# Kernel tuning notes

Hardware: AMD Instinct MI355X
Metric: run time of the kernel (lower is better)

Reference implementation:

```python
import jax, jax.numpy as jnp
import numpy as np

N = 100000
C = 64
E = 3200000


def setup_inputs() -> dict:
    key = jax.random.key(0)
    k1, k2, k3 = jax.random.split(key, 3)
    edge_index = jax.random.randint(k1, (2, E), 0, N, dtype=jnp.int64)
    # nn.Linear(num_nodes, out_channels): weight [C, N], bias [C]
    W = jax.random.normal(k2, (C, N), dtype=jnp.float32) * 0.01
    b = jax.random.normal(k3, (C,), dtype=jnp.float32) * 0.01
    return {"edge_index": edge_index, "W": W, "b": b}


def reference(edge_index, W, b):
    # logits = A @ W.T + b, with A the N x N COO adjacency built from edge_index.
    # Row r of A @ W.T = sum_{edges (r, c)} W[:, c], so this is a gather of
    # W.T rows at col, segment-summed over row (duplicate edges accumulate,
    # matching torch sparse COO semantics).
    n = W.shape[1]
    row = edge_index[0]
    col = edge_index[1]
    row = row - row.min()  # faithful to the original's row normalization
    Wt = W.T  # [N, C]
    gathered = Wt[col]  # [E, C]
    out = jax.ops.segment_sum(gathered, row, num_segments=n)  # [N, C]
    return out + b
```

## Files before the change

### kernel.cpp

```cpp
#include <hip/hip_runtime.h>


#define OVF_MAX (1 << 19)
#define NBKT_MAX 400
#define SLOTS 36
#define FLUSH_T 24
#define GT_STRIDE 16
#define SL 64

__device__ __forceinline__ float bf16u_to_f(unsigned short u) {
    union { unsigned int i; float f; } x; x.i = ((unsigned int)u) << 16; return x.f;
}

__global__ __launch_bounds__(1024) void LINK_detect_kernel(
    const unsigned int* __restrict__ words, int E, int* __restrict__ flags,
    int* __restrict__ gtail, int nbkt, int segcap) {
    long long twoE = 2LL * E;
    int tid = threadIdx.x;
    unsigned int oddOr = 0u;
    int nscan = (int)(twoE < 8192 ? twoE : 8192);
    for (int i = tid; i < nscan; i += blockDim.x) {
        if (i & 1) oddOr |= words[i];
        long long j = twoE - 1 - i;
        if (j >= nscan && (j & 1)) oddOr |= words[j];
    }
    __shared__ unsigned int sred[16];
    for (int off = 32; off > 0; off >>= 1)
        oddOr |= (unsigned int)__shfl_down((int)oddOr, off, 64);
    int wid = tid >> 6;
    if ((tid & 63) == 0) sred[wid] = oddOr;
    __syncthreads();
    if (tid == 0) {
        unsigned int o = 0;
        for (int i = 0; i < (int)(blockDim.x >> 6); ++i) o |= sred[i];
        flags[0] = o ? 1 : 0;
        flags[1] = 0x7fffffff;
        flags[8] = 0;
    }
    for (int k = tid; k < nbkt; k += blockDim.x) gtail[k * GT_STRIDE] = k * segcap;
}

__global__ void LINK_transpose_kernel(const float* __restrict__ W,
                                      unsigned short* __restrict__ Wtb, int N) {
    __shared__ float tile[64][65];
    int n0 = blockIdx.x * 64;
    int lx = threadIdx.x & 63;
    int ly = threadIdx.x >> 6;
#pragma unroll
    for (int it = 0; it < 16; ++it) {
        int ch = ly + 4 * it;
        float v = 0.0f;
        if (n0 + lx < N) v = W[(size_t)ch * N + (n0 + lx)];
        tile[lx][ch] = v;
    }
    __syncthreads();
#pragma unroll
    for (int it = 0; it < 16; ++it) {
        int nn = ly + 4 * it;
        if (n0 + nn < N) {
            union { float f; unsigned int i; } x; x.f = tile[nn][lx];
            unsigned int u = x.i;
            unsigned int r = (u + 0x7fffu + ((u >> 16) & 1u)) >> 16;
            Wtb[((size_t)(n0 + nn) << 6) + lx] = (unsigned short)r;
        }
    }
}

__global__ __launch_bounds__(1024) void LINK_part_kernel(
    const unsigned int* __restrict__ words, int E, int N, int nbkt, int segcap,
    int* __restrict__ gtail, unsigned int* __restrict__ recs,
    int* __restrict__ ovf, int* __restrict__ flags) {
    __shared__ unsigned int lstage[NBKT_MAX * SLOTS];
    __shared__ int lcnt[NBKT_MAX];
    __shared__ int sred[16];
    int tid = threadIdx.x;
    for (int k = tid; k < nbkt; k += blockDim.x) lcnt[k] = 0;
    __syncthreads();
    int isInt32 = flags[0];
    int mnr = 0x7fffffff;
    int nblk = gridDim.x;
    long long per_round = (long long)nblk * blockDim.x;
    long long nround = ((long long)E + per_round - 1) / per_round;
    int lane = tid & 63, wid = tid >> 6, nw = blockDim.x >> 6;
    for (long long rd = 0; rd < nround; ++rd) {
        long long e = (rd * nblk + blockIdx.x) * blockDim.x + tid;
        if (e < E) {
            int r, c;
            if (isInt32) {
                r = (int)__builtin_nontemporal_load(words + e);
                c = (int)__builtin_nontemporal_load(words + E + e);
            } else {
                r = (int)__builtin_nontemporal_load(words + 2 * e);
                c = (int)__builtin_nontemporal_load(words + 2LL * E + 2 * e);
            }
            mnr = min(mnr, r);
            if ((unsigned)r < (unsigned)N && (unsigned)c < (unsigned)N) {
                int k = r >> 8;
                unsigned int rec = ((unsigned int)(r & 255) << 17) | (unsigned int)c;
                int pos = atomicAdd(&lcnt[k], 1);
                if (pos < SLOTS) {
                    lstage[k * SLOTS + pos] = rec;
                } else {
                    int g = atomicAdd(&gtail[k * GT_STRIDE], 1);
                    if (g < (k + 1) * segcap) recs[g] = rec;
                    else {
                        int oi = atomicAdd(&flags[8], 1);
                        if (oi < OVF_MAX) { ovf[2 * oi] = r; ovf[2 * oi + 1] = c; }
                    }
                }
            }
        }
        __syncthreads();
        bool last = (rd == nround - 1);
        for (int k = wid; k < nbkt; k += nw) {
            int cnt = lcnt[k]; if (cnt > SLOTS) cnt = SLOTS;
            if (cnt >= FLUSH_T || (last && cnt > 0)) {
                int g = 0;
                if (lane == 0) g = atomicAdd(&gtail[k * GT_STRIDE], cnt);
                g = __shfl(g, 0);
                if (lane < cnt) {
                    int gg = g + lane;
                    unsigned int rec = lstage[k * SLOTS + lane];
                    if (gg < (k + 1) * segcap) recs[gg] = rec;
                    else {
                        int oi = atomicAdd(&flags[8], 1);
                        if (oi < OVF_MAX) {
                            ovf[2 * oi] = (k << 8) | (int)(rec >> 17);
                            ovf[2 * oi + 1] = (int)(rec & 0x1FFFF);
                        }
                    }
                }
                if (lane == 0) lcnt[k] = 0;
            }
        }
        __syncthreads();
    }
    for (int off = 32; off > 0; off >>= 1) mnr = min(mnr, __shfl_down(mnr, off, 64));
    if (lane == 0) sred[wid] = mnr;
    __syncthreads();
    if (tid == 0) {
        int m = 0x7fffffff;
        for (int i = 0; i < 16; ++i) m = min(m, sred[i]);
        atomicMin(&flags[1], m);
    }
}

__global__ __launch_bounds__(256, 8) void LINK_bgather_kernel(
    const int* __restrict__ gtail, const unsigned int* __restrict__ recs, int segcap,
    const unsigned short* __restrict__ Wtb, const float* __restrict__ bias,
    float* __restrict__ out, int* __restrict__ flags, int* __restrict__ ovf, int N) {
    __shared__ int lcols[64 * SL];
    __shared__ int lcnt[64];
    int b = blockIdx.x >> 2;
    int sub = blockIdx.x & 3;
    int tid = threadIdx.x;
    if (tid < 64) lcnt[tid] = 0;
    __syncthreads();
    int len = gtail[b * GT_STRIDE] - b * segcap;
    if (len > segcap) len = segcap;
    if (len < 0) len = 0;
    const unsigned int* rp = recs + (size_t)b * segcap;
    for (int i = tid; i < len; i += 256) {
        unsigned int rec = rp[i];
        int lrf = (int)(rec >> 17);
        if ((lrf >> 6) != sub) continue;
        int lr = lrf & 63;
        int c = (int)(rec & 0x1FFFF);
        int pos = atomicAdd(&lcnt[lr], 1);
        if (pos < SL) {
            lcols[(lr << 6) + pos] = c;
        } else {
            int oi = atomicAdd(&flags[8], 1);
            if (oi < OVF_MAX) { ovf[2 * oi] = (b << 8) | lrf; ovf[2 * oi + 1] = c; }
        }
    }
    __syncthreads();
    int rmin = flags[1];
    int lane = tid & 63, wid = tid >> 6;
    for (int lr = wid; lr < 64; lr += 4) {
        int cnt = lcnt[lr]; if (cnt > SL) cnt = SL;
        int base = lr << 6;
        float acc = 0.0f;
        int j = 0;
        for (; j + 16 <= cnt; j += 16) {
            int c0 = lcols[base + j + 0], c1 = lcols[base + j + 1];
            int c2 = lcols[base + j + 2], c3 = lcols[base + j + 3];
            int c4 = lcols[base + j + 4], c5 = lcols[base + j + 5];
            int c6 = lcols[base + j + 6], c7 = lcols[base + j + 7];
            int c8 = lcols[base + j + 8], c9 = lcols[base + j + 9];
            int cA = lcols[base + j + 10], cB = lcols[base + j + 11];
            int cC = lcols[base + j + 12], cD = lcols[base + j + 13];
            int cE = lcols[base + j + 14], cF = lcols[base + j + 15];
            unsigned short u0 = Wtb[((size_t)c0 << 6) + lane];
            unsigned short u1 = Wtb[((size_t)c1 << 6) + lane];
            unsigned short u2 = Wtb[((size_t)c2 << 6) + lane];
            unsigned short u3 = Wtb[((size_t)c3 << 6) + lane];
            unsigned short u4 = Wtb[((size_t)c4 << 6) + lane];
            unsigned short u5 = Wtb[((size_t)c5 << 6) + lane];
            unsigned short u6 = Wtb[((size_t)c6 << 6) + lane];
            unsigned short u7 = Wtb[((size_t)c7 << 6) + lane];
            unsigned short u8 = Wtb[((size_t)c8 << 6) + lane];
            unsigned short u9 = Wtb[((size_t)c9 << 6) + lane];
            unsigned short uA = Wtb[((size_t)cA << 6) + lane];
            unsigned short uB = Wtb[((size_t)cB << 6) + lane];
            unsigned short uC = Wtb[((size_t)cC << 6) + lane];
            unsigned short uD = Wtb[((size_t)cD << 6) + lane];
            unsigned short uE = Wtb[((size_t)cE << 6) + lane];
            unsigned short uF = Wtb[((size_t)cF << 6) + lane];
            float s0 = (bf16u_to_f(u0) + bf16u_to_f(u1)) + (bf16u_to_f(u2) + bf16u_to_f(u3));
            float s1 = (bf16u_to_f(u4) + bf16u_to_f(u5)) + (bf16u_to_f(u6) + bf16u_to_f(u7));
            float s2 = (bf16u_to_f(u8) + bf16u_to_f(u9)) + (bf16u_to_f(uA) + bf16u_to_f(uB));
            float s3 = (bf16u_to_f(uC) + bf16u_to_f(uD)) + (bf16u_to_f(uE) + bf16u_to_f(uF));
            acc += (s0 + s1) + (s2 + s3);
        }
        for (; j + 8 <= cnt; j += 8) {
            int c0 = lcols[base + j + 0], c1 = lcols[base + j + 1];
            int c2 = lcols[base + j + 2], c3 = lcols[base + j + 3];
            int c4 = lcols[base + j + 4], c5 = lcols[base + j + 5];
            int c6 = lcols[base + j + 6], c7 = lcols[base + j + 7];
            unsigned short u0 = Wtb[((size_t)c0 << 6) + lane];
            unsigned short u1 = Wtb[((size_t)c1 << 6) + lane];
            unsigned short u2 = Wtb[((size_t)c2 << 6) + lane];
            unsigned short u3 = Wtb[((size_t)c3 << 6) + lane];
            unsigned short u4 = Wtb[((size_t)c4 << 6) + lane];
            unsigned short u5 = Wtb[((size_t)c5 << 6) + lane];
            unsigned short u6 = Wtb[((size_t)c6 << 6) + lane];
            unsigned short u7 = Wtb[((size_t)c7 << 6) + lane];
            float s0 = (bf16u_to_f(u0) + bf16u_to_f(u1)) + (bf16u_to_f(u2) + bf16u_to_f(u3));
            float s1 = (bf16u_to_f(u4) + bf16u_to_f(u5)) + (bf16u_to_f(u6) + bf16u_to_f(u7));
            acc += s0 + s1;
        }
        for (; j < cnt; ++j)
            acc += bf16u_to_f(Wtb[((size_t)lcols[base + j] << 6) + lane]);
        int orow = (b << 8) + (sub << 6) + lr - rmin;
        if ((unsigned)orow < (unsigned)N)
            out[((size_t)orow << 6) + lane] = acc + bias[lane];
    }
}

__global__ void LINK_biastail_kernel(float* __restrict__ out, const float* __restrict__ bias,
                                     const int* __restrict__ flags, int N, int nbkt) {
    int rmin = flags[1];
    long long start = (long long)nbkt * 256 - (long long)rmin;
    if (start < 0) start = 0;
    if (start >= N) return;
    long long total = ((long long)N - start) * 64;
    long long base = start * 64;
    long long i0 = (long long)blockIdx.x * blockDim.x + threadIdx.x;
    long long stride = (long long)gridDim.x * blockDim.x;
    for (long long i = i0; i < total; i += stride) out[base + i] = bias[(int)(i & 63)];
}

__global__ void LINK_ovf_kernel(const int* __restrict__ ovf, const int* __restrict__ flags,
                                const unsigned short* __restrict__ Wtb,
                                float* __restrict__ out, int N) {
    int g = blockIdx.x * blockDim.x + threadIdx.x;
    int w = g >> 6, lane = g & 63;
    int cnt = flags[8]; if (cnt > OVF_MAX) cnt = OVF_MAX;
    if (cnt == 0) return;
    int rmin = flags[1];
    int nw = (gridDim.x * blockDim.x) >> 6;
    for (int i = w; i < cnt; i += nw) {
        int r = ovf[2 * i] - rmin;
        int c = ovf[2 * i + 1];
        if ((unsigned)r >= (unsigned)N || (unsigned)c >= (unsigned)N) continue;
        atomicAdd(&out[((size_t)r << 6) + lane], bf16u_to_f(Wtb[((size_t)c << 6) + lane]));
    }
}

__global__ void LINK_initout_kernel(float* __restrict__ out, const float* __restrict__ b,
                                    int total, int* __restrict__ flags) {
    int i = blockIdx.x * blockDim.x + threadIdx.x;
    if (i == 0) { flags[0] = 0; flags[1] = 0x7fffffff; flags[2] = 0x7fffffff; }
    if (i < total) out[i] = b[i & 63];
}

__global__ __launch_bounds__(256) void LINK_analyze_kernel(
    const unsigned int* __restrict__ words, int E, int* __restrict__ flags) {
    const uint4* __restrict__ w4 = (const uint4*)words;
    int tid = blockIdx.x * blockDim.x + threadIdx.x;
    int nth = gridDim.x * blockDim.x;
    int n1 = E >> 2;
    long long twoE = 2LL * E;
    int n2 = (int)(twoE >> 2);
    unsigned int oddOr = 0u;
    int mn32 = 0x7fffffff, mn64 = 0x7fffffff;
    for (int i = tid; i < n2; i += nth) {
        uint4 w = w4[i];
        oddOr |= (w.y | w.w);
        mn64 = min(mn64, min((int)w.x, (int)w.z));
        if (i < n1)
            mn32 = min(mn32, min(min((int)w.x, (int)w.y), min((int)w.z, (int)w.w)));
    }
    for (long long i = ((long long)n1 << 2) + tid; i < E; i += nth)
        mn32 = min(mn32, (int)words[i]);
    for (long long i = ((long long)n2 << 2) + tid; i < twoE; i += nth) {
        unsigned int w = words[i];
        if (i & 1) oddOr |= w; else mn64 = min(mn64, (int)w);
    }
    for (int off = 32; off > 0; off >>= 1) {
        oddOr |= (unsigned int)__shfl_down((int)oddOr, off, 64);
        mn32 = min(mn32, __shfl_down(mn32, off, 64));
        mn64 = min(mn64, __shfl_down(mn64, off, 64));
    }
    __shared__ int s_or[4], s_m32[4], s_m64[4];
    int wid = threadIdx.x >> 6;
    if ((threadIdx.x & 63) == 0) { s_or[wid] = (int)oddOr; s_m32[wid] = mn32; s_m64[wid] = mn64; }
    __syncthreads();
    if (threadIdx.x == 0) {
        int o = s_or[0] | s_or[1] | s_or[2] | s_or[3];
        int a = min(min(s_m32[0], s_m32[1]), min(s_m32[2], s_m32[3]));
        int d = min(min(s_m64[0], s_m64[1]), min(s_m64[2], s_m64[3]));
        if (o) atomicOr(&flags[0], 1);
        atomicMin(&flags[1], a);
        atomicMin(&flags[2], d);
    }
}

__global__ void LINK_scatter_kernel(const unsigned int* __restrict__ words, int E,
                                    const float* __restrict__ W,
                                    float* __restrict__ out,
                                    const int* __restrict__ flags, int N) {
    long long g = (long long)blockIdx.x * blockDim.x + threadIdx.x;
    int e = (int)(g >> 6);
    if (e >= E) return;
    int ch = (int)(g & 63);
    int r, c, rmin;
    if (flags[0]) { r = (int)words[e]; c = (int)words[E + e]; rmin = flags[1]; }
    else { r = (int)words[2LL * e]; c = (int)words[2LL * (E + e)]; rmin = flags[2]; }
    r -= rmin;
    if ((unsigned)r >= (unsigned)N || (unsigned)c >= (unsigned)N) return;
    atomicAdd(&out[((size_t)r << 6) + ch], W[(size_t)ch * N + c]);
}

static inline size_t align256(size_t x) { return (x + 255) & ~(size_t)255; }

extern "C" void kernel_launch(void* const* d_in, const int* in_sizes, int n_in,
                              void* d_out, int out_size, void* d_ws, size_t ws_size,
                              hipStream_t stream) {
    const unsigned int* words = (const unsigned int*)d_in[0];
    const float* W = (const float*)d_in[1];
    const float* b = (const float*)d_in[2];
    float* out = (float*)d_out;

    int E = in_sizes[0] / 2;
    int N = in_sizes[1] / 64;
    int total = out_size;
    int nbkt = (N + 255) / 256;

    size_t off_flags = 0;
    size_t off_wtb   = align256(off_flags + 256 * sizeof(int));
    size_t off_gtail = align256(off_wtb + (size_t)N * 64 * sizeof(unsigned short));
    size_t off_ovf   = align256(off_gtail + (size_t)NBKT_MAX * GT_STRIDE * sizeof(int));
    size_t off_recs  = align256(off_ovf + (size_t)OVF_MAX * 2 * sizeof(int));

    int* flags = (int*)((char*)d_ws + off_flags);
    unsigned short* Wtb = (unsigned short*)((char*)d_ws + off_wtb);
    int* gtail = (int*)((char*)d_ws + off_gtail);
    int* ovf   = (int*)((char*)d_ws + off_ovf);
    unsigned int* recs = (unsigned int*)((char*)d_ws + off_recs);

    long long avail = (ws_size > off_recs)
        ? (long long)((ws_size - off_recs) / ((size_t)nbkt * sizeof(int))) : 0;
    int segcap = (int)(avail > 16384 ? 16384 : avail);
    int avg = (int)((long long)E / (nbkt > 0 ? nbkt : 1)) + 1;
    bool useMain = (N <= (1 << 17)) && (nbkt <= NBKT_MAX) &&
                   (segcap >= avg + avg / 4 + SLOTS) && (E > 0);

    if (useMain) {
        LINK_detect_kernel<<<1, 1024, 0, stream>>>(words, E, flags, gtail, nbkt, segcap);
        LINK_transpose_kernel<<<(N + 63) / 64, 256, 0, stream>>>(W, Wtb, N);
        LINK_part_kernel<<<512, 1024, 0, stream>>>(words, E, N, nbkt, segcap,
                                                   gtail, recs, ovf, flags);
        LINK_bgather_kernel<<<nbkt * 4, 256, 0, stream>>>(gtail, recs, segcap, Wtb, b,
                                                          out, flags, ovf, N);
        LINK_biastail_kernel<<<64, 256, 0, stream>>>(out, b, flags, N, nbkt);
        LINK_ovf_kernel<<<64, 256, 0, stream>>>(ovf, flags, Wtb, out, N);
    } else {
        LINK_initout_kernel<<<(total + 255) / 256, 256, 0, stream>>>(out, b, total, flags);
        LINK_analyze_kernel<<<256, 256, 0, stream>>>(words, E, flags);
        long long tthreads = (long long)E * 64;
        LINK_scatter_kernel<<<(int)((tthreads + 255) / 256), 256, 0, stream>>>(
            words, E, W, out, flags, N);
    }
}
```

Measured before the change: 226.1 us.

## Gather two bf16 channels per lane with split half-wave edge processing

Rewrites the bucketed gather so each lane loads a 32-bit word holding two bf16 channels, with the two half-waves handling alternate edges and combining through a cross-half shuffle. Column lists are read from LDS as int4/int2 vectors and padded to even length with a sentinel zero row appended to the transposed weight table. Blocks now hold 512 threads covering 128 rows instead of 256 threads covering 64, which halves the number of passes over each bucket's records. The aim is fewer, wider global load instructions and less redundant record scanning, at the cost of larger shared memory per block and an extra shuffle reduction per row.

```diff
diff --git a/kernel.cpp b/kernel.cpp
--- a/kernel.cpp
+++ b/kernel.cpp
@@ -10,6 +10,12 @@
 
 __device__ __forceinline__ float bf16u_to_f(unsigned short u) {
     union { unsigned int i; float f; } x; x.i = ((unsigned int)u) << 16; return x.f;
+}
+__device__ __forceinline__ float bflo(unsigned int u) {
+    union { unsigned int i; float f; } x; x.i = u << 16; return x.f;
+}
+__device__ __forceinline__ float bfhi(unsigned int u) {
+    union { unsigned int i; float f; } x; x.i = u & 0xFFFF0000u; return x.f;
 }
 
 __global__ __launch_bounds__(1024) void LINK_detect_kernel(
@@ -57,7 +63,7 @@
 #pragma unroll
     for (int it = 0; it < 16; ++it) {
         int nn = ly + 4 * it;
-        if (n0 + nn < N) {
+        if (n0 + nn <= N) {
             union { float f; unsigned int i; } x; x.f = tile[nn][lx];
             unsigned int u = x.i;
             unsigned int r = (u + 0x7fffu + ((u >> 16) & 1u)) >> 16;
@@ -145,26 +151,26 @@
     }
 }
 
-__global__ __launch_bounds__(256, 8) void LINK_bgather_kernel(
+__global__ __launch_bounds__(512, 8) void LINK_bgather_kernel(
     const int* __restrict__ gtail, const unsigned int* __restrict__ recs, int segcap,
     const unsigned short* __restrict__ Wtb, const float* __restrict__ bias,
     float* __restrict__ out, int* __restrict__ flags, int* __restrict__ ovf, int N) {
-    __shared__ int lcols[64 * SL];
-    __shared__ int lcnt[64];
-    int b = blockIdx.x >> 2;
-    int sub = blockIdx.x & 3;
+    __shared__ __attribute__((aligned(16))) int lcols[128 * SL];
+    __shared__ int lcnt[128];
+    int b = blockIdx.x >> 1;
+    int sub = blockIdx.x & 1;
     int tid = threadIdx.x;
-    if (tid < 64) lcnt[tid] = 0;
+    if (tid < 128) lcnt[tid] = 0;
     __syncthreads();
     int len = gtail[b * GT_STRIDE] - b * segcap;
     if (len > segcap) len = segcap;
     if (len < 0) len = 0;
     const unsigned int* rp = recs + (size_t)b * segcap;
-    for (int i = tid; i < len; i += 256) {
+    for (int i = tid; i < len; i += 512) {
         unsigned int rec = rp[i];
         int lrf = (int)(rec >> 17);
-        if ((lrf >> 6) != sub) continue;
-        int lr = lrf & 63;
+        if ((lrf >> 7) != sub) continue;
+        int lr = lrf & 127;
         int c = (int)(rec & 0x1FFFF);
         int pos = atomicAdd(&lcnt[lr], 1);
         if (pos < SL) {
@@ -175,66 +181,67 @@
         }
     }
     __syncthreads();
+    if (tid < 128) {
+        int c0 = lcnt[tid]; if (c0 > SL) c0 = SL;
+        if (c0 & 1) { lcols[(tid << 6) + c0] = N; ++c0; }
+        lcnt[tid] = c0;
+    }
+    __syncthreads();
     int rmin = flags[1];
     int lane = tid & 63, wid = tid >> 6;
-    for (int lr = wid; lr < 64; lr += 4) {
-        int cnt = lcnt[lr]; if (cnt > SL) cnt = SL;
+    int half = lane >> 5, ln = lane & 31;
+    const unsigned int* __restrict__ W32 = (const unsigned int*)Wtb;
+    float bv = bias[(ln << 1) + half];
+    for (int lr = wid; lr < 128; lr += 8) {
+        int cnt = lcnt[lr];
         int base = lr << 6;
-        float acc = 0.0f;
+        float aL = 0.0f, aH = 0.0f;
         int j = 0;
         for (; j + 16 <= cnt; j += 16) {
-            int c0 = lcols[base + j + 0], c1 = lcols[base + j + 1];
-            int c2 = lcols[base + j + 2], c3 = lcols[base + j + 3];
-            int c4 = lcols[base + j + 4], c5 = lcols[base + j + 5];
-            int c6 = lcols[base + j + 6], c7 = lcols[base + j + 7];
-            int c8 = lcols[base + j + 8], c9 = lcols[base + j + 9];
-            int cA = lcols[base + j + 10], cB = lcols[base + j + 11];
-            int cC = lcols[base + j + 12], cD = lcols[base + j + 13];
-            int cE = lcols[base + j + 14], cF = lcols[base + j + 15];
-            unsigned short u0 = Wtb[((size_t)c0 << 6) + lane];
-            unsigned short u1 = Wtb[((size_t)c1 << 6) + lane];
-            unsigned short u2 = Wtb[((size_t)c2 << 6) + lane];
-            unsigned short u3 = Wtb[((size_t)c3 << 6) + lane];
-            unsigned short u4 = Wtb[((size_t)c4 << 6) + lane];
-            unsigned short u5 = Wtb[((size_t)c5 << 6) + lane];
-            unsigned short u6 = Wtb[((size_t)c6 << 6) + lane];
-            unsigned short u7 = Wtb[((size_t)c7 << 6) + lane];
-            unsigned short u8 = Wtb[((size_t)c8 << 6) + lane];
-            unsigned short u9 = Wtb[((size_t)c9 << 6) + lane];
-            unsigned short uA = Wtb[((size_t)cA << 6) + lane];
-            unsigned short uB = Wtb[((size_t)cB << 6) + lane];
-            unsigned short uC = Wtb[((size_t)cC << 6) + lane];
-            unsigned short uD = Wtb[((size_t)cD << 6) + lane];
-            unsigned short uE = Wtb[((size_t)cE << 6) + lane];
-            unsigned short uF = Wtb[((size_t)cF << 6) + lane];
-            float s0 = (bf16u_to_f(u0) + bf16u_to_f(u1)) + (bf16u_to_f(u2) + bf16u_to_f(u3));
-            float s1 = (bf16u_to_f(u4) + bf16u_to_f(u5)) + (bf16u_to_f(u6) + bf16u_to_f(u7));
-            float s2 = (bf16u_to_f(u8) + bf16u_to_f(u9)) + (bf16u_to_f(uA) + bf16u_to_f(uB));
-            float s3 = (bf16u_to_f(uC) + bf16u_to_f(uD)) + (bf16u_to_f(uE) + bf16u_to_f(uF));
-            acc += (s0 + s1) + (s2 + s3);
+            int4 q0 = *(const int4*)&lcols[base + j + (half << 2)];
+            int4 q1 = *(const int4*)&lcols[base + j + 8 + (half << 2)];
+            unsigned int u0 = W32[(((unsigned)q0.x) << 5) | ln];
+            unsigned int u1 = W32[(((unsigned)q0.y) << 5) | ln];
+            unsigned int u2 = W32[(((unsigned)q0.z) << 5) | ln];
+            unsigned int u3 = W32[(((unsigned)q0.w) << 5) | ln];
+            unsigned int u4 = W32[(((unsigned)q1.x) << 5) | ln];
+            unsigned int u5 = W32[(((unsigned)q1.y) << 5) | ln];
+            unsigned int u6 = W32[(((unsigned)q1.z) << 5) | ln];
+            unsigned int u7 = W32[(((unsigned)q1.w) << 5) | ln];
+            float l0 = (bflo(u0) + bflo(u1)) + (bflo(u2) + bflo(u3));
+            float l1 = (bflo(u4) + bflo(u5)) + (bflo(u6) + bflo(u7));
+            float h0 = (bfhi(u0) + bfhi(u1)) + (bfhi(u2) + bfhi(u3));
+            float h1 = (bfhi(u4) + bfhi(u5)) + (bfhi(u6) + bfhi(u7));
+            aL += l0 + l1;
+            aH += h0 + h1;
         }
         for (; j + 8 <= cnt; j += 8) {
-            int c0 = lcols[base + j + 0], c1 = lcols[base + j + 1];
-            int c2 = lcols[base + j + 2], c3 = lcols[base + j + 3];
-            int c4 = lcols[base + j + 4], c5 = lcols[base + j + 5];
-            int c6 = lcols[base + j + 6], c7 = lcols[base + j + 7];
-            unsigned short u0 = Wtb[((size_t)c0 << 6) + lane];
-            unsigned short u1 = Wtb[((size_t)c1 << 6) + lane];
-            unsigned short u2 = Wtb[((size_t)c2 << 6) + lane];
-            unsigned short u3 = Wtb[((size_t)c3 << 6) + lane];
-            unsigned short u4 = Wtb[((size_t)c4 << 6) + lane];
-            unsigned short u5 = Wtb[((size_t)c5 << 6) + lane];
-            unsigned short u6 = Wtb[((size_t)c6 << 6) + lane];
-            unsigned short u7 = Wtb[((size_t)c7 << 6) + lane];
-            float s0 = (bf16u_to_f(u0) + bf16u_to_f(u1)) + (bf16u_to_f(u2) + bf16u_to_f(u3));
-            float s1 = (bf16u_to_f(u4) + bf16u_to_f(u5)) + (bf16u_to_f(u6) + bf16u_to_f(u7));
-            acc += s0 + s1;
-        }
-        for (; j < cnt; ++j)
-            acc += bf16u_to_f(Wtb[((size_t)lcols[base + j] << 6) + lane]);
-        int orow = (b << 8) + (sub << 6) + lr - rmin;
+            int4 q = *(const int4*)&lcols[base + j + (half << 2)];
+            unsigned int u0 = W32[(((unsigned)q.x) << 5) | ln];
+            unsigned int u1 = W32[(((unsigned)q.y) << 5) | ln];
+            unsigned int u2 = W32[(((unsigned)q.z) << 5) | ln];
+            unsigned int u3 = W32[(((unsigned)q.w) << 5) | ln];
+            aL += (bflo(u0) + bflo(u1)) + (bflo(u2) + bflo(u3));
+            aH += (bfhi(u0) + bfhi(u1)) + (bfhi(u2) + bfhi(u3));
+        }
+        for (; j + 4 <= cnt; j += 4) {
+            int2 q = *(const int2*)&lcols[base + j + (half << 1)];
+            unsigned int u0 = W32[(((unsigned)q.x) << 5) | ln];
+            unsigned int u1 = W32[(((unsigned)q.y) << 5) | ln];
+            aL += bflo(u0) + bflo(u1);
+            aH += bfhi(u0) + bfhi(u1);
+        }
+        for (; j + 2 <= cnt; j += 2) {
+            int c = lcols[base + j + half];
+            unsigned int u = W32[(((unsigned)c) << 5) | ln];
+            aL += bflo(u);
+            aH += bfhi(u);
+        }
+        aL += __shfl_xor(aL, 32, 64);
+        aH += __shfl_xor(aH, 32, 64);
+        int orow = (b << 8) + (sub << 7) + lr - rmin;
         if ((unsigned)orow < (unsigned)N)
-            out[((size_t)orow << 6) + lane] = acc + bias[lane];
+            out[((size_t)orow << 6) + (ln << 1) + half] = (half ? aH : aL) + bv;
     }
 }
 
@@ -350,7 +357,7 @@
 
     size_t off_flags = 0;
     size_t off_wtb   = align256(off_flags + 256 * sizeof(int));
-    size_t off_gtail = align256(off_wtb + (size_t)N * 64 * sizeof(unsigned short));
+    size_t off_gtail = align256(off_wtb + (size_t)(N + 1) * 64 * sizeof(unsigned short));
     size_t off_ovf   = align256(off_gtail + (size_t)NBKT_MAX * GT_STRIDE * sizeof(int));
     size_t off_recs  = align256(off_ovf + (size_t)OVF_MAX * 2 * sizeof(int));
 
@@ -369,10 +376,10 @@
 
     if (useMain) {
         LINK_detect_kernel<<<1, 1024, 0, stream>>>(words, E, flags, gtail, nbkt, segcap);
-        LINK_transpose_kernel<<<(N + 63) / 64, 256, 0, stream>>>(W, Wtb, N);
+        LINK_transpose_kernel<<<(N + 64) / 64, 256, 0, stream>>>(W, Wtb, N);
         LINK_part_kernel<<<512, 1024, 0, stream>>>(words, E, N, nbkt, segcap,
                                                    gtail, recs, ovf, flags);
-        LINK_bgather_kernel<<<nbkt * 4, 256, 0, stream>>>(gtail, recs, segcap, Wtb, b,
+        LINK_bgather_kernel<<<nbkt * 2, 512, 0, stream>>>(gtail, recs, segcap, Wtb, b,
                                                           out, flags, ovf, N);
         LINK_biastail_kernel<<<64, 256, 0, stream>>>(out, b, flags, N, nbkt);
         LINK_ovf_kernel<<<64, 256, 0, stream>>>(ovf, flags, Wtb, out, N);
```

Result: faster. 210.9 us (-6.7%).
